# Optimization experiments

Hardware: AMD Instinct MI355X
Metric: run time of the kernel (lower is better)

Reference implementation:

```python
import jax, jax.numpy as jnp
import numpy as np

CONF_TH = 0.25   # default conf_thresh in non_max_suppression
NMS_TH = 0.35    # default nms_thresh


def setup_inputs() -> dict:
    key = jax.random.key(0)
    # [N, C=5+num_classes, H, W]
    preds = jax.random.normal(key, (64, 85, 32, 32), dtype=jnp.float32)
    return {"preds": preds}


def _decode(preds):
    """Faithful box decode: [N,C,H,W] -> [N, H*W, 6] (x1,y1,x2,y2,score,cls)."""
    N, C, H, W = preds.shape
    p = jnp.transpose(preds, (0, 2, 3, 1))           # [N,H,W,C]
    pobj = p[..., 0]
    preg = p[..., 1:5]
    pcls = p[..., 5:]
    score = pobj * jnp.max(pcls, axis=-1)             # obj * max-class
    cls = jax.lax.stop_gradient(jnp.argmax(pcls, axis=-1).astype(preds.dtype))
    gy, gx = jnp.meshgrid(jnp.arange(H, dtype=preds.dtype),
                          jnp.arange(W, dtype=preds.dtype), indexing="ij")
    bw = jax.nn.sigmoid(preg[..., 2])
    bh = jax.nn.sigmoid(preg[..., 3])
    bcx = (jnp.tanh(preg[..., 0]) + gx) / W
    bcy = (jnp.tanh(preg[..., 1]) + gy) / H
    x1 = bcx - 0.5 * bw
    y1 = bcy - 0.5 * bh
    x2 = bcx + 0.5 * bw
    y2 = bcy + 0.5 * bh
    bboxes = jnp.stack([x1, y1, x2, y2, score, cls], axis=-1)  # [N,H,W,6]
    return bboxes.reshape(N, H * W, 6)


def _iou_matrix(boxes):
    """[M,4] xyxy -> [M,M] pairwise IoU."""
    x1, y1, x2, y2 = boxes[:, 0], boxes[:, 1], boxes[:, 2], boxes[:, 3]
    area = (x2 - x1) * (y2 - y1)
    iw = jnp.clip(jnp.minimum(x2[:, None], x2[None, :]) - jnp.maximum(x1[:, None], x1[None, :]), 0.0)
    ih = jnp.clip(jnp.minimum(y2[:, None], y2[None, :]) - jnp.maximum(y1[:, None], y1[None, :]), 0.0)
    inter = iw * ih
    return inter / (area[:, None] + area[None, :] - inter + 1e-9)


def _nms_single(bb):
    """Greedy class-aware NMS on one image's [M,6] boxes.
    Equivalent to: filter score>CONF_TH then torchvision.batched_nms.
    Returns keep mask [M] in the original box order (fixed shape)."""
    M = bb.shape[0]
    order = jnp.argsort(-bb[:, 4])                    # descending score
    b = bb[order]
    iou = _iou_matrix(b[:, :4])
    same_cls = b[:, 5][:, None] == b[:, 5][None, :]
    supp_mat = (iou > NMS_TH) & same_cls              # [M,M]
    valid_s = b[:, 4] > CONF_TH

    def body(i, keep):
        suppressed = jnp.any(keep & supp_mat[i])
        return keep.at[i].set(valid_s[i] & ~suppressed)

    keep_s = jax.lax.fori_loop(0, M, body, jnp.zeros((M,), jnp.bool_))
    # scatter back to original order
    return jnp.zeros((M,), jnp.bool_).at[order].set(keep_s)


def reference(preds):
    bboxes = _decode(preds)                # [N, HW, 6]
    keep = jax.vmap(_nms_single)(bboxes)   # [N, HW] bool keep mask
    return bboxes, keep
```

## Files before the change

### kernel.cpp

```cpp
#include <hip/hip_runtime.h>
#include <math.h>

#define NIMG 64
#define HW   1024
#define NCH  85
#define NCLS 80
#define CONF_TH 0.25f
#define NMS_TH  0.35f

__device__ __forceinline__ float fast_tanh(float x) {
  float e = __expf(2.0f * x);
  return 1.0f - 2.0f * __builtin_amdgcn_rcpf(e + 1.0f);
}
__device__ __forceinline__ float fast_sigmoid(float x) {
  return __builtin_amdgcn_rcpf(1.0f + __expf(-x));
}

__global__ __launch_bounds__(256) void decode_kernel(const float* __restrict__ preds,
                                                     float* __restrict__ out) {
  int g = blockIdx.x * 256 + threadIdx.x;
  int t = g & (HW - 1);
  const float* base = preds + (size_t)(g >> 10) * (NCH * HW) + t;

  float pobj = base[0];
  float tx = base[1 * HW], ty = base[2 * HW];
  float tw = base[3 * HW], th = base[4 * HW];

  float b0 = base[5 * HW], b1 = base[6 * HW], b2 = base[7 * HW], b3 = base[8 * HW];
  int i0 = 0, i1 = 1, i2 = 2, i3 = 3;
#pragma unroll
  for (int c = 4; c < NCLS; c += 4) {
    float v0 = base[(5 + c) * HW];
    float v1 = base[(6 + c) * HW];
    float v2 = base[(7 + c) * HW];
    float v3 = base[(8 + c) * HW];
    if (v0 > b0) { b0 = v0; i0 = c; }
    if (v1 > b1) { b1 = v1; i1 = c + 1; }
    if (v2 > b2) { b2 = v2; i2 = c + 2; }
    if (v3 > b3) { b3 = v3; i3 = c + 3; }
  }
  float best = b0; int bc = i0;
  if (b1 > best || (b1 == best && i1 < bc)) { best = b1; bc = i1; }
  if (b2 > best || (b2 == best && i2 < bc)) { best = b2; bc = i2; }
  if (b3 > best || (b3 == best && i3 < bc)) { best = b3; bc = i3; }

  float score = pobj * best;

  float gx = (float)(t & 31);
  float gy = (float)(t >> 5);
  float bcx = (fast_tanh(tx) + gx) * 0.03125f;
  float bcy = (fast_tanh(ty) + gy) * 0.03125f;
  float bw = fast_sigmoid(tw);
  float bh = fast_sigmoid(th);

  float x1 = bcx - 0.5f * bw, y1 = bcy - 0.5f * bh;
  float x2 = bcx + 0.5f * bw, y2 = bcy + 0.5f * bh;

  float2* ob = (float2*)(out + (size_t)g * 6);
  ob[0] = make_float2(x1, y1);
  ob[1] = make_float2(x2, y2);
  ob[2] = make_float2(score, (float)bc);
}

__global__ __launch_bounds__(256) void nms_kernel(const float* __restrict__ bboxes,
                                                  float* __restrict__ keepOut) {
  int n = blockIdx.x;
  int t = threadIdx.x;

  __shared__ float sx1[HW], sy1[HW], sx2[HW], sy2[HW], sarea[HW], sscore[HW];
  __shared__ int scls[HW];
  __shared__ int bucket[HW];
  __shared__ int sorted[HW];
  __shared__ int srank[HW];
  __shared__ unsigned long long supp[HW];
  __shared__ int cnt[NCLS], offs[NCLS], start[NCLS];

  if (t < NCLS) cnt[t] = 0;
  __syncthreads();

#pragma unroll
  for (int k = 0; k < 4; ++k) {
    int px = t + 256 * k;
    size_t gb = (size_t)n * HW + px;
    const float2* bb = (const float2*)(bboxes + gb * 6);
    float2 p0 = bb[0], p1 = bb[1], p2 = bb[2];
    keepOut[gb] = 0.0f;
    sx1[px] = p0.x; sy1[px] = p0.y; sx2[px] = p1.x; sy2[px] = p1.y;
    sarea[px] = (p1.x - p0.x) * (p1.y - p0.y);
    sscore[px] = p2.x;
    int cls = (int)p2.y;
    scls[px] = cls;
    if (p2.x > CONF_TH) atomicAdd(&cnt[cls], 1);
  }
  __syncthreads();

  if (t < 64) {
    int c0 = (2 * t < NCLS) ? cnt[2 * t] : 0;
    int c1 = (2 * t + 1 < NCLS) ? cnt[2 * t + 1] : 0;
    int ps = c0 + c1;
    int x = ps;
#pragma unroll
    for (int d = 1; d < 64; d <<= 1) {
      int y = __shfl_up(x, d, 64);
      if (t >= d) x += y;
    }
    int excl = x - ps;
    if (2 * t < NCLS)     { start[2 * t] = excl;      offs[2 * t] = excl; }
    if (2 * t + 1 < NCLS) { start[2 * t + 1] = excl + c0; offs[2 * t + 1] = excl + c0; }
  }
  __syncthreads();

#pragma unroll
  for (int k = 0; k < 4; ++k) {
    int px = t + 256 * k;
    if (sscore[px] > CONF_TH) {
      int p = atomicAdd(&offs[scls[px]], 1);
      bucket[p] = px;
    }
  }
  __syncthreads();

#pragma unroll
  for (int k = 0; k < 4; ++k) {
    int px = t + 256 * k;
    float s = sscore[px];
    if (s > CONF_TH) {
      int c = scls[px], s0 = start[c], m = cnt[c];
      int r = 0;
      for (int j = 0; j < m; ++j) {
        int jb = bucket[s0 + j];
        float sj = sscore[jb];
        r += (sj > s) || (sj == s && jb < px);
      }
      srank[px] = r;
      sorted[s0 + r] = px;
    }
  }
  __syncthreads();

#pragma unroll
  for (int k = 0; k < 4; ++k) {
    int px = t + 256 * k;
    float s = sscore[px];
    if (s > CONF_TH) {
      int c = scls[px], s0 = start[c];
      int a = srank[px];
      int lim = a < 64 ? a : 64;
      float ax1 = sx1[px], ay1 = sy1[px], ax2 = sx2[px], ay2 = sy2[px];
      float aar = sarea[px];
      unsigned long long mask = 0ull;
      for (int b = 0; b < lim; ++b) {
        int jb = sorted[s0 + b];
        float iw = fminf(ax2, sx2[jb]) - fmaxf(ax1, sx1[jb]);
        float ih = fminf(ay2, sy2[jb]) - fmaxf(ay1, sy1[jb]);
        iw = fmaxf(iw, 0.0f);
        ih = fmaxf(ih, 0.0f);
        float inter = iw * ih;
        float iou = inter / (aar + sarea[jb] - inter + 1e-9f);
        if (iou > NMS_TH) mask |= (1ull << b);
      }
      supp[s0 + a] = mask;
    }
  }
  __syncthreads();

  if (t < NCLS) {
    int m = cnt[t], s0 = start[t];
    if (m <= 64) {
      unsigned long long kept = 0ull;
      for (int a = 0; a < m; ++a) {
        unsigned long long sa = supp[s0 + a];
        if ((sa & kept) == 0ull) {
          kept |= (1ull << a);
          keepOut[(size_t)n * HW + sorted[s0 + a]] = 1.0f;
        }
      }
    } else {
      for (int a = 0; a < m; ++a) {
        int ia = sorted[s0 + a];
        float ax1 = sx1[ia], ay1 = sy1[ia], ax2 = sx2[ia], ay2 = sy2[ia];
        float aar = sarea[ia];
        bool kp = true;
        for (int b = 0; b < a; ++b) {
          if (!bucket[s0 + b]) continue;
          int jb = sorted[s0 + b];
          float iw = fminf(ax2, sx2[jb]) - fmaxf(ax1, sx1[jb]);
          float ih = fminf(ay2, sy2[jb]) - fmaxf(ay1, sy1[jb]);
          iw = fmaxf(iw, 0.0f);
          ih = fmaxf(ih, 0.0f);
          float inter = iw * ih;
          float iou = inter / (aar + sarea[jb] - inter + 1e-9f);
          if (iou > NMS_TH) { kp = false; break; }
        }
        bucket[s0 + a] = kp ? 1 : 0;
        if (kp) keepOut[(size_t)n * HW + ia] = 1.0f;
      }
    }
  }
}

extern "C" void kernel_launch(void* const* d_in, const int* in_sizes, int n_in,
                              void* d_out, int out_size, void* d_ws, size_t ws_size,
                              hipStream_t stream) {
  const float* preds = (const float*)d_in[0];
  float* out = (float*)d_out;
  float* keepOut = out + (size_t)NIMG * HW * 6;

  decode_kernel<<<(NIMG * HW) / 256, 256, 0, stream>>>(preds, out);
  nms_kernel<<<NIMG, 256, 0, stream>>>(out, keepOut);
}
```

Baseline: 82.96 us.

## Fuse decode and NMS into one per-image kernel with 1024 threads

Merges the decode kernel and the NMS kernel into a single kernel that launches one 1024-thread block per image. Each thread decodes one box and writes it to shared memory directly, so NMS no longer re-reads the decoded boxes from global memory. This also removes one kernel launch. The cost is that decode now runs on only 64 blocks, which reduces parallelism for the memory-bound decode read of the predictions.

```diff
diff --git a/kernel.cpp b/kernel.cpp
--- a/kernel.cpp
+++ b/kernel.cpp
@@ -16,11 +16,23 @@
   return __builtin_amdgcn_rcpf(1.0f + __expf(-x));
 }
 
-__global__ __launch_bounds__(256) void decode_kernel(const float* __restrict__ preds,
-                                                     float* __restrict__ out) {
-  int g = blockIdx.x * 256 + threadIdx.x;
-  int t = g & (HW - 1);
-  const float* base = preds + (size_t)(g >> 10) * (NCH * HW) + t;
+__global__ __launch_bounds__(1024) void fused_kernel(const float* __restrict__ preds,
+                                                     float* __restrict__ out,
+                                                     float* __restrict__ keepOut) {
+  int n = blockIdx.x;
+  int t = threadIdx.x;
+
+  __shared__ float sx1[HW], sy1[HW], sx2[HW], sy2[HW], sarea[HW], sscore[HW];
+  __shared__ int scls[HW];
+  __shared__ int bucket[HW];
+  __shared__ int sorted[HW];
+  __shared__ int srank[HW];
+  __shared__ unsigned long long supp[HW];
+  __shared__ int cnt[NCLS], offs[NCLS], start[NCLS];
+
+  if (t < NCLS) cnt[t] = 0;
+
+  const float* base = preds + (size_t)n * (NCH * HW) + t;
 
   float pobj = base[0];
   float tx = base[1 * HW], ty = base[2 * HW];
@@ -56,42 +68,21 @@
   float x1 = bcx - 0.5f * bw, y1 = bcy - 0.5f * bh;
   float x2 = bcx + 0.5f * bw, y2 = bcy + 0.5f * bh;
 
-  float2* ob = (float2*)(out + (size_t)g * 6);
+  size_t gb = (size_t)n * HW + t;
+  float2* ob = (float2*)(out + gb * 6);
   ob[0] = make_float2(x1, y1);
   ob[1] = make_float2(x2, y2);
   ob[2] = make_float2(score, (float)bc);
-}
 
-__global__ __launch_bounds__(256) void nms_kernel(const float* __restrict__ bboxes,
-                                                  float* __restrict__ keepOut) {
-  int n = blockIdx.x;
-  int t = threadIdx.x;
-
-  __shared__ float sx1[HW], sy1[HW], sx2[HW], sy2[HW], sarea[HW], sscore[HW];
-  __shared__ int scls[HW];
-  __shared__ int bucket[HW];
-  __shared__ int sorted[HW];
-  __shared__ int srank[HW];
-  __shared__ unsigned long long supp[HW];
-  __shared__ int cnt[NCLS], offs[NCLS], start[NCLS];
-
-  if (t < NCLS) cnt[t] = 0;
+  sx1[t] = x1; sy1[t] = y1; sx2[t] = x2; sy2[t] = y2;
+  sarea[t] = (x2 - x1) * (y2 - y1);
+  sscore[t] = score;
+  scls[t] = bc;
+  bool valid = score > CONF_TH;
   __syncthreads();
 
-#pragma unroll
-  for (int k = 0; k < 4; ++k) {
-    int px = t + 256 * k;
-    size_t gb = (size_t)n * HW + px;
-    const float2* bb = (const float2*)(bboxes + gb * 6);
-    float2 p0 = bb[0], p1 = bb[1], p2 = bb[2];
-    keepOut[gb] = 0.0f;
-    sx1[px] = p0.x; sy1[px] = p0.y; sx2[px] = p1.x; sy2[px] = p1.y;
-    sarea[px] = (p1.x - p0.x) * (p1.y - p0.y);
-    sscore[px] = p2.x;
-    int cls = (int)p2.y;
-    scls[px] = cls;
-    if (p2.x > CONF_TH) atomicAdd(&cnt[cls], 1);
-  }
+  keepOut[gb] = 0.0f;
+  if (valid) atomicAdd(&cnt[bc], 1);
   __syncthreads();
 
   if (t < 64) {
@@ -105,62 +96,47 @@
       if (t >= d) x += y;
     }
     int excl = x - ps;
-    if (2 * t < NCLS)     { start[2 * t] = excl;      offs[2 * t] = excl; }
+    if (2 * t < NCLS)     { start[2 * t] = excl;          offs[2 * t] = excl; }
     if (2 * t + 1 < NCLS) { start[2 * t + 1] = excl + c0; offs[2 * t + 1] = excl + c0; }
   }
   __syncthreads();
 
-#pragma unroll
-  for (int k = 0; k < 4; ++k) {
-    int px = t + 256 * k;
-    if (sscore[px] > CONF_TH) {
-      int p = atomicAdd(&offs[scls[px]], 1);
-      bucket[p] = px;
-    }
+  if (valid) {
+    int p = atomicAdd(&offs[bc], 1);
+    bucket[p] = t;
   }
   __syncthreads();
 
-#pragma unroll
-  for (int k = 0; k < 4; ++k) {
-    int px = t + 256 * k;
-    float s = sscore[px];
-    if (s > CONF_TH) {
-      int c = scls[px], s0 = start[c], m = cnt[c];
-      int r = 0;
-      for (int j = 0; j < m; ++j) {
-        int jb = bucket[s0 + j];
-        float sj = sscore[jb];
-        r += (sj > s) || (sj == s && jb < px);
-      }
-      srank[px] = r;
-      sorted[s0 + r] = px;
+  if (valid) {
+    int s0 = start[bc], m = cnt[bc];
+    int r = 0;
+    for (int j = 0; j < m; ++j) {
+      int jb = bucket[s0 + j];
+      float sj = sscore[jb];
+      r += (sj > score) || (sj == score && jb < t);
     }
+    srank[t] = r;
+    sorted[s0 + r] = t;
   }
   __syncthreads();
 
-#pragma unroll
-  for (int k = 0; k < 4; ++k) {
-    int px = t + 256 * k;
-    float s = sscore[px];
-    if (s > CONF_TH) {
-      int c = scls[px], s0 = start[c];
-      int a = srank[px];
-      int lim = a < 64 ? a : 64;
-      float ax1 = sx1[px], ay1 = sy1[px], ax2 = sx2[px], ay2 = sy2[px];
-      float aar = sarea[px];
-      unsigned long long mask = 0ull;
-      for (int b = 0; b < lim; ++b) {
-        int jb = sorted[s0 + b];
-        float iw = fminf(ax2, sx2[jb]) - fmaxf(ax1, sx1[jb]);
-        float ih = fminf(ay2, sy2[jb]) - fmaxf(ay1, sy1[jb]);
-        iw = fmaxf(iw, 0.0f);
-        ih = fmaxf(ih, 0.0f);
-        float inter = iw * ih;
-        float iou = inter / (aar + sarea[jb] - inter + 1e-9f);
-        if (iou > NMS_TH) mask |= (1ull << b);
-      }
-      supp[s0 + a] = mask;
+  if (valid) {
+    int s0 = start[bc];
+    int a = srank[t];
+    int lim = a < 64 ? a : 64;
+    unsigned long long mask = 0ull;
+    for (int b = 0; b < lim; ++b) {
+      int jb = sorted[s0 + b];
+      float iw = fminf(x2, sx2[jb]) - fmaxf(x1, sx1[jb]);
+      float ih = fminf(y2, sy2[jb]) - fmaxf(y1, sy1[jb]);
+      iw = fmaxf(iw, 0.0f);
+      ih = fmaxf(ih, 0.0f);
+      float inter = iw * ih;
+      float aar = (x2 - x1) * (y2 - y1);
+      float iou = inter / (aar + sarea[jb] - inter + 1e-9f);
+      if (iou > NMS_TH) mask |= (1ull << b);
     }
+    supp[s0 + a] = mask;
   }
   __syncthreads();
 
@@ -206,6 +182,5 @@
   float* out = (float*)d_out;
   float* keepOut = out + (size_t)NIMG * HW * 6;
 
-  decode_kernel<<<(NIMG * HW) / 256, 256, 0, stream>>>(preds, out);
-  nms_kernel<<<NIMG, 256, 0, stream>>>(out, keepOut);
+  fused_kernel<<<NIMG, HW, 0, stream>>>(preds, out, keepOut);
 }
```

New measurement: 82.07 us. About the same (-1.1%).
